# Kernel optimization log

Hardware: AMD Instinct MI355X
Metric: run time of the kernel (lower is better)

The kernel has to match this reference:

```python
import jax, jax.numpy as jnp
import numpy as np

B, H, W, C = 32, 256, 256, 4
KH, KW, F = 5, 5, 8


def setup_inputs() -> dict:
    key = jax.random.key(0)
    kx, kk = jax.random.split(key)
    x = jax.random.normal(kx, (B, H, W, C), dtype=jnp.float32)
    kernel = jax.random.normal(kk, (KH, KW, C, F), dtype=jnp.float32) * 0.1
    return {"x": x, "kernel": kernel}


def reference(x, kernel):
    """Multi-filter grayscale erosion (min-plus correlation), channels-last.

    out[b, y, x, f] = min_{dy, dx, c} ( x[b, y+dy, x+dx, c] - kernel[dy, dx, c, f] )
    (stride 1, VALID padding, rates 1 -- matching tf.nn.erosion2d followed by
    a min-reduction over the input-channel axis, per output filter.)
    """
    kh, kw, c, f = kernel.shape
    b, h, w, _ = x.shape
    ho, wo = h - kh + 1, w - kw + 1  # VALID output size
    out = None
    # Fixed, small structural loop over the kh*kw window taps; each tap is a
    # fully vectorized shifted slice + min-plus reduction over channels.
    for i in range(kh):
        for j in range(kw):
            patch = x[:, i:i + ho, j:j + wo, :]                      # [B,Ho,Wo,C]
            # min over channels of (patch - kernel tap): [B,Ho,Wo,F]
            v = jnp.min(patch[..., :, None] - kernel[i, j][None, None, None, :, :], axis=3)
            out = v if out is None else jnp.minimum(out, v)
    return out
```

## Files before the change

### kernel.cpp

```cpp
#include <hip/hip_runtime.h>

#define BB 32
#define HH 256
#define WW 256
#define CC 4
#define KH 5
#define KW 5
#define FF 8
#define HO (HH - KH + 1)
#define WO (WW - KW + 1)
#define PX 4
#define NXT (WO / PX)
#define NCOL (PX + KW - 1)

typedef _Float16 h2     __attribute__((ext_vector_type(2)));
typedef __fp16   fp16x2 __attribute__((ext_vector_type(2)));

static __device__ __forceinline__ h2 pkrtz(float a, float b) {
    fp16x2 r = __builtin_amdgcn_cvt_pkrtz(a, b);
    return __builtin_bit_cast(h2, r);
}

__global__ void pack_kernel(const float* __restrict__ k, unsigned int* __restrict__ kp)
{
    int i = blockIdx.x * blockDim.x + threadIdx.x;
    if (i >= KH * KW * FF * 2) return;
    int t = i >> 4;
    int r = i & 15;
    int f = r >> 1;
    int p = r & 1;
    float a = k[(t * CC + 2 * p + 0) * FF + f];
    float b = k[(t * CC + 2 * p + 1) * FF + f];
    kp[i] = __builtin_bit_cast(unsigned int, pkrtz(a, b));
}

__global__ __launch_bounds__(256, 3) void erosion2d_f16(
    const float* __restrict__ x,
    const h2* __restrict__ k2,
    float* __restrict__ out)
{
    const int total = BB * HO * NXT;
    int tid = blockIdx.x * blockDim.x + threadIdx.x;
    if (tid >= total) return;

    int b   = tid / (HO * NXT);
    int rem = tid - b * (HO * NXT);
    int y   = rem / NXT;
    int xt  = rem - y * NXT;
    const int x0 = xt * PX;

    const float* xb = x + (((size_t)b * HH + y) * WW + x0) * CC;

    h2 pc[KH][NCOL][2];
#pragma unroll
    for (int r = 0; r < KH; ++r) {
#pragma unroll
        for (int j = 0; j < NCOL; ++j) {
            const float4 px = *reinterpret_cast<const float4*>(xb + (r * WW + j) * CC);
            pc[r][j][0] = pkrtz(px.x, px.y);
            pc[r][j][1] = pkrtz(px.z, px.w);
        }
    }

    h2 acc[PX][FF];
    const h2 big = { (_Float16)65504.0f, (_Float16)65504.0f };
#pragma unroll
    for (int p = 0; p < PX; ++p)
#pragma unroll
        for (int f = 0; f < FF; ++f)
            acc[p][f] = big;

#pragma unroll
    for (int dy = 0; dy < KH; ++dy) {
#pragma unroll
        for (int dx = 0; dx < KW; ++dx) {
            const h2* kt = k2 + (dy * KW + dx) * (FF * 2);
#pragma unroll
            for (int p = 0; p < PX; ++p) {
                const h2 c01 = pc[dy][dx + p][0];
                const h2 c23 = pc[dy][dx + p][1];
#pragma unroll
                for (int f = 0; f < FF; ++f) {
                    h2 d01 = c01 - kt[f * 2 + 0];
                    h2 d23 = c23 - kt[f * 2 + 1];
                    acc[p][f] = __builtin_elementwise_min(
                        acc[p][f], __builtin_elementwise_min(d01, d23));
                }
            }
        }
    }

#pragma unroll
    for (int p = 0; p < PX; ++p) {
        float r[FF];
#pragma unroll
        for (int f = 0; f < FF; ++f)
            r[f] = fminf((float)acc[p][f][0], (float)acc[p][f][1]);
        float* op = out + (((size_t)b * HO + y) * WO + (x0 + p)) * FF;
        *reinterpret_cast<float4*>(op)     = make_float4(r[0], r[1], r[2], r[3]);
        *reinterpret_cast<float4*>(op + 4) = make_float4(r[4], r[5], r[6], r[7]);
    }
}

extern "C" void kernel_launch(void* const* d_in, const int* in_sizes, int n_in,
                              void* d_out, int out_size, void* d_ws, size_t ws_size,
                              hipStream_t stream) {
    const float* x = (const float*)d_in[0];
    const float* k = (const float*)d_in[1];
    float* out = (float*)d_out;

    pack_kernel<<<2, 256, 0, stream>>>(k, (unsigned int*)d_ws);

    const int total = BB * HO * NXT;
    const int block = 256;
    const int grid  = (total + block - 1) / block;
    erosion2d_f16<<<grid, block, 0, stream>>>(x, (const h2*)d_ws, out);
}
```

Before: 70.85 us.

## Fuse kernel packing into LDS, stream input rows, halve pixels per thread

Drops the separate weight-pack launch: each block converts the kernel to packed fp16 in shared memory and reads each tap's weights with vector LDS loads. The full 5-row input window is no longer held in registers; rows are loaded one at a time and the next row's load is issued before the current row's compute. Pixels per thread drop from 4 to 2, and the occupancy hint is removed. The aim is lower register pressure, higher occupancy and one fewer launch, at the cost of more redundant input loads across overlapping columns and per-block weight packing.

```diff
diff --git a/kernel.cpp b/kernel.cpp
--- a/kernel.cpp
+++ b/kernel.cpp
@@ -9,36 +9,40 @@
 #define FF 8
 #define HO (HH - KH + 1)
 #define WO (WW - KW + 1)
-#define PX 4
+#define PX 2
 #define NXT (WO / PX)
 #define NCOL (PX + KW - 1)
 
 typedef _Float16 h2     __attribute__((ext_vector_type(2)));
 typedef __fp16   fp16x2 __attribute__((ext_vector_type(2)));
+typedef unsigned int u32x4 __attribute__((ext_vector_type(4)));
 
 static __device__ __forceinline__ h2 pkrtz(float a, float b) {
     fp16x2 r = __builtin_amdgcn_cvt_pkrtz(a, b);
     return __builtin_bit_cast(h2, r);
 }
-
-__global__ void pack_kernel(const float* __restrict__ k, unsigned int* __restrict__ kp)
-{
-    int i = blockIdx.x * blockDim.x + threadIdx.x;
-    if (i >= KH * KW * FF * 2) return;
-    int t = i >> 4;
-    int r = i & 15;
-    int f = r >> 1;
-    int p = r & 1;
-    float a = k[(t * CC + 2 * p + 0) * FF + f];
-    float b = k[(t * CC + 2 * p + 1) * FF + f];
-    kp[i] = __builtin_bit_cast(unsigned int, pkrtz(a, b));
+static __device__ __forceinline__ h2 ash2(unsigned int u) {
+    return __builtin_bit_cast(h2, u);
 }
 
-__global__ __launch_bounds__(256, 3) void erosion2d_f16(
+__global__ __launch_bounds__(256) void erosion2d_f16(
     const float* __restrict__ x,
-    const h2* __restrict__ k2,
+    const float* __restrict__ k,
     float* __restrict__ out)
 {
+    __shared__ unsigned int lw[KH * KW * 16];
+
+    for (int i = threadIdx.x; i < KH * KW * 16; i += 256) {
+        int t = i >> 4;
+        int r = i & 15;
+        int f = r >> 1;
+        int p = r & 1;
+        float a = k[(t * CC + 2 * p + 0) * FF + f];
+        float b = k[(t * CC + 2 * p + 1) * FF + f];
+        lw[i] = __builtin_bit_cast(unsigned int, pkrtz(a, b));
+    }
+    __syncthreads();
+
     const int total = BB * HO * NXT;
     int tid = blockIdx.x * blockDim.x + threadIdx.x;
     if (tid >= total) return;
@@ -51,17 +55,6 @@
 
     const float* xb = x + (((size_t)b * HH + y) * WW + x0) * CC;
 
-    h2 pc[KH][NCOL][2];
-#pragma unroll
-    for (int r = 0; r < KH; ++r) {
-#pragma unroll
-        for (int j = 0; j < NCOL; ++j) {
-            const float4 px = *reinterpret_cast<const float4*>(xb + (r * WW + j) * CC);
-            pc[r][j][0] = pkrtz(px.x, px.y);
-            pc[r][j][1] = pkrtz(px.z, px.w);
-        }
-    }
-
     h2 acc[PX][FF];
     const h2 big = { (_Float16)65504.0f, (_Float16)65504.0f };
 #pragma unroll
@@ -70,19 +63,46 @@
         for (int f = 0; f < FF; ++f)
             acc[p][f] = big;
 
+    float4 raw[NCOL];
+    h2 cur[NCOL][2];
+
 #pragma unroll
-    for (int dy = 0; dy < KH; ++dy) {
+    for (int j = 0; j < NCOL; ++j)
+        raw[j] = *reinterpret_cast<const float4*>(xb + j * CC);
+
+#pragma unroll
+    for (int r = 0; r < KH; ++r) {
+#pragma unroll
+        for (int j = 0; j < NCOL; ++j) {
+            cur[j][0] = pkrtz(raw[j].x, raw[j].y);
+            cur[j][1] = pkrtz(raw[j].z, raw[j].w);
+        }
+        if (r + 1 < KH) {
+#pragma unroll
+            for (int j = 0; j < NCOL; ++j)
+                raw[j] = *reinterpret_cast<const float4*>(xb + ((r + 1) * WW + j) * CC);
+        }
 #pragma unroll
         for (int dx = 0; dx < KW; ++dx) {
-            const h2* kt = k2 + (dy * KW + dx) * (FF * 2);
+            const u32x4* q = reinterpret_cast<const u32x4*>(&lw[(r * KW + dx) * 16]);
+            u32x4 q0 = q[0], q1 = q[1], q2 = q[2], q3 = q[3];
+            h2 w01[FF], w23[FF];
+            w01[0] = ash2(q0[0]); w23[0] = ash2(q0[1]);
+            w01[1] = ash2(q0[2]); w23[1] = ash2(q0[3]);
+            w01[2] = ash2(q1[0]); w23[2] = ash2(q1[1]);
+            w01[3] = ash2(q1[2]); w23[3] = ash2(q1[3]);
+            w01[4] = ash2(q2[0]); w23[4] = ash2(q2[1]);
+            w01[5] = ash2(q2[2]); w23[5] = ash2(q2[3]);
+            w01[6] = ash2(q3[0]); w23[6] = ash2(q3[1]);
+            w01[7] = ash2(q3[2]); w23[7] = ash2(q3[3]);
 #pragma unroll
             for (int p = 0; p < PX; ++p) {
-                const h2 c01 = pc[dy][dx + p][0];
-                const h2 c23 = pc[dy][dx + p][1];
+                const h2 c01 = cur[dx + p][0];
+                const h2 c23 = cur[dx + p][1];
 #pragma unroll
                 for (int f = 0; f < FF; ++f) {
-                    h2 d01 = c01 - kt[f * 2 + 0];
-                    h2 d23 = c23 - kt[f * 2 + 1];
+                    h2 d01 = c01 - w01[f];
+                    h2 d23 = c23 - w23[f];
                     acc[p][f] = __builtin_elementwise_min(
                         acc[p][f], __builtin_elementwise_min(d01, d23));
                 }
@@ -92,13 +112,15 @@
 
 #pragma unroll
     for (int p = 0; p < PX; ++p) {
-        float r[FF];
+        float rr[FF];
 #pragma unroll
-        for (int f = 0; f < FF; ++f)
-            r[f] = fminf((float)acc[p][f][0], (float)acc[p][f][1]);
-        float* op = out + (((size_t)b * HO + y) * WO + (x0 + p)) * FF;
-        *reinterpret_cast<float4*>(op)     = make_float4(r[0], r[1], r[2], r[3]);
-        *reinterpret_cast<float4*>(op + 4) = make_float4(r[4], r[5], r[6], r[7]);
+        for (int f = 0; f < FF; ++f) {
+            _Float16 m = __builtin_elementwise_min(acc[p][f][0], acc[p][f][1]);
+            rr[f] = (float)m;
+        }
+        float* op = out + ((size_t)tid * PX + p) * FF;
+        *reinterpret_cast<float4*>(op)     = make_float4(rr[0], rr[1], rr[2], rr[3]);
+        *reinterpret_cast<float4*>(op + 4) = make_float4(rr[4], rr[5], rr[6], rr[7]);
     }
 }
 
@@ -109,10 +131,8 @@
     const float* k = (const float*)d_in[1];
     float* out = (float*)d_out;
 
-    pack_kernel<<<2, 256, 0, stream>>>(k, (unsigned int*)d_ws);
-
     const int total = BB * HO * NXT;
     const int block = 256;
     const int grid  = (total + block - 1) / block;
-    erosion2d_f16<<<grid, block, 0, stream>>>(x, (const h2*)d_ws, out);
+    erosion2d_f16<<<grid, block, 0, stream>>>(x, k, out);
 }
```

After: 61.38 us. 13.4% less time.
